# Kernel tuning notes

Hardware: AMD Instinct MI355X
Metric: run time of the kernel (lower is better)

Reference implementation:

```python
import jax, jax.numpy as jnp
import numpy as np

ALPHA = 0.9
BETA = 0.85
THRESHOLD = 0.1
SURR_SCALE = 100.0  # SpyTorch-style surrogate gradient scale


@jax.custom_vjp
def surr_spike(x):
    # Heaviside forward, surrogate gradient backward (SurrGradSpike)
    return (x > 0.0).astype(x.dtype)


def _surr_fwd(x):
    return surr_spike(x), x


def _surr_bwd(x, g):
    return (g / (SURR_SCALE * jnp.abs(x) + 1.0) ** 2,)


surr_spike.defvjp(_surr_fwd, _surr_bwd)


def setup_inputs() -> dict:
    key = jax.random.key(0)
    k1, k2, k3 = jax.random.split(key, 3)
    B, T, D_IN, N = 64, 256, 512, 1024
    inputs = jax.random.normal(k1, (B, T, D_IN), dtype=jnp.float32)
    weights = 0.1 * jax.random.normal(k2, (D_IN, N), dtype=jnp.float32)
    recurrent_weights = 0.1 * jax.random.normal(k3, (N, N), dtype=jnp.float32)
    return {"inputs": inputs, "weights": weights, "recurrent_weights": recurrent_weights}


def reference(inputs, weights, recurrent_weights):
    B, T, D_IN = inputs.shape
    N = weights.shape[1]

    def step(carry, x_t):
        mem, syn, spk = carry
        h = jnp.einsum('bd,dn->bn', x_t, weights)          # input projection
        rec_h = jnp.einsum('bn,nm->bm', spk, recurrent_weights)  # recurrent drive
        new_syn = ALPHA * syn + h + rec_h
        new_mem = BETA * mem + new_syn
        mthr = new_mem - THRESHOLD
        out = surr_spike(mthr)
        new_mem = jnp.where(mthr > 0.0, jnp.zeros_like(new_mem), new_mem)  # reset
        return (new_mem, new_syn, out), (out, new_mem, new_syn)

    zeros = jnp.zeros((B, N), dtype=inputs.dtype)
    init = (zeros, zeros, zeros)
    x_tbd = jnp.transpose(inputs, (1, 0, 2))  # [T, B, D]
    (mem, syn, spk), (spk_rec, mem_rec, syn_rec) = jax.lax.scan(step, init, x_tbd)
    # back to [B, T, N]
    spk_rec = jnp.transpose(spk_rec, (1, 0, 2))
    mem_rec = jnp.transpose(mem_rec, (1, 0, 2))
    syn_rec = jnp.transpose(syn_rec, (1, 0, 2))
    return (spk_rec, (mem, syn, spk), (mem_rec, syn_rec))
```

## Files before the change

### kernel.cpp

```cpp
#include <hip/hip_runtime.h>

typedef __attribute__((ext_vector_type(8))) _Float16 f16x8;
typedef __attribute__((ext_vector_type(4))) float f32x4;

static constexpr int   B_  = 64;
static constexpr int   T_  = 256;
static constexpr int   D_  = 512;
static constexpr int   N_  = 1024;
static constexpr float ALPHA_ = 0.9f;
static constexpr float BETA_  = 0.85f;
static constexpr float THR_   = 0.1f;
static constexpr float INV4096 = 1.0f / 4096.0f;

__global__ __launch_bounds__(256) void dsrnn_wsplit(const float* __restrict__ W,
                                                    unsigned char* __restrict__ Wfrag) {
  const int u    = blockIdx.x * 256 + threadIdx.x;
  const int lane = u & 63;
  const int bi   = u >> 6;
  const int cf   = bi >> 4;
  const int chk  = bi & 15;
  const int kg   = lane >> 4;
  const int cc   = lane & 15;
  const int n    = cf * 16 + cc;
  const int k0   = chk * 32 + kg * 8;
  f16x8 vh, vl;
#pragma unroll
  for (int j = 0; j < 8; ++j) {
    const float v = W[(size_t)(k0 + j) * N_ + n];
    const _Float16 h = (_Float16)v;
    vh[j] = h;
    vl[j] = (_Float16)((v - (float)h) * 4096.0f);
  }
  unsigned char* dst = Wfrag + (size_t)bi * 2048 + lane * 16;
  *reinterpret_cast<f16x8*>(dst)        = vh;
  *reinterpret_cast<f16x8*>(dst + 1024) = vl;
}

__global__ __launch_bounds__(256) void dsrnn_hgemm2(const float* __restrict__ X,
                                                    const unsigned char* __restrict__ Wfrag,
                                                    float* __restrict__ H) {
  __shared__ __align__(16) _Float16 Xa_hi[64][40];
  __shared__ __align__(16) _Float16 Xa_lo[64][40];
  const int tid  = threadIdx.x;
  const int rb   = blockIdx.x >> 3;
  const int nb   = (blockIdx.x & 7) << 7;
  const int r0   = rb << 6;
  const int wv   = tid >> 6;
  const int lane = tid & 63;
  const int kg   = lane >> 4;
  const int cc   = lane & 15;

  f32x4 ah[4][2], am[4][2];
#pragma unroll
  for (int i = 0; i < 4; ++i)
#pragma unroll
    for (int j = 0; j < 2; ++j) {
      ah[i][j] = (f32x4){0.f, 0.f, 0.f, 0.f};
      am[i][j] = (f32x4){0.f, 0.f, 0.f, 0.f};
    }

  const int srow = tid >> 2;
  const int skq  = (tid & 3) << 3;

  for (int kc = 0; kc < 16; ++kc) {
    {
      const float* xp = X + (size_t)(r0 + srow) * D_ + kc * 32 + skq;
      const float4 v0 = *reinterpret_cast<const float4*>(xp);
      const float4 v1 = *reinterpret_cast<const float4*>(xp + 4);
      const float vv[8] = {v0.x, v0.y, v0.z, v0.w, v1.x, v1.y, v1.z, v1.w};
      f16x8 xh, xl;
#pragma unroll
      for (int j = 0; j < 8; ++j) {
        const _Float16 h = (_Float16)vv[j];
        xh[j] = h;
        xl[j] = (_Float16)((vv[j] - (float)h) * 4096.0f);
      }
      *reinterpret_cast<f16x8*>(&Xa_hi[srow][skq]) = xh;
      *reinterpret_cast<f16x8*>(&Xa_lo[srow][skq]) = xl;
    }
    __syncthreads();

    f16x8 Bh[2], Bl[2];
#pragma unroll
    for (int cfi = 0; cfi < 2; ++cfi) {
      const unsigned char* bp =
          Wfrag + (size_t)((((nb >> 4) + (wv << 1) + cfi) * 16 + kc) * 2048) + lane * 16;
      Bh[cfi] = *reinterpret_cast<const f16x8*>(bp);
      Bl[cfi] = *reinterpret_cast<const f16x8*>(bp + 1024);
    }

#pragma unroll
    for (int rf = 0; rf < 4; ++rf) {
      const f16x8 Ah = *reinterpret_cast<const f16x8*>(&Xa_hi[rf * 16 + cc][kg * 8]);
      const f16x8 Al = *reinterpret_cast<const f16x8*>(&Xa_lo[rf * 16 + cc][kg * 8]);
#pragma unroll
      for (int cfi = 0; cfi < 2; ++cfi) {
        ah[rf][cfi] = __builtin_amdgcn_mfma_f32_16x16x32_f16(Ah, Bh[cfi], ah[rf][cfi], 0, 0, 0);
        am[rf][cfi] = __builtin_amdgcn_mfma_f32_16x16x32_f16(Ah, Bl[cfi], am[rf][cfi], 0, 0, 0);
        am[rf][cfi] = __builtin_amdgcn_mfma_f32_16x16x32_f16(Al, Bh[cfi], am[rf][cfi], 0, 0, 0);
      }
    }
    __syncthreads();
  }

#pragma unroll
  for (int rf = 0; rf < 4; ++rf)
#pragma unroll
    for (int cfi = 0; cfi < 2; ++cfi) {
      const int col = nb + wv * 32 + cfi * 16 + cc;
#pragma unroll
      for (int rr = 0; rr < 4; ++rr) {
        const int row = r0 + rf * 16 + kg * 4 + rr;
        H[(size_t)row * N_ + col] = fmaf(am[rf][cfi][rr], INV4096, ah[rf][cfi][rr]);
      }
    }
}

__global__ __launch_bounds__(256, 1) void dsrnn_step10(
    const float* __restrict__ Rw,
    float* __restrict__ spk_rec,
    float* __restrict__ mem_rec,
    float* __restrict__ syn_rec,
    float* __restrict__ mem_fin,
    float* __restrict__ syn_fin,
    float* __restrict__ spk_fin,
    unsigned long long* masks)
{
  extern __shared__ unsigned char RsB[];
  __shared__ unsigned smaskU[16][33];
  __shared__ float scratch[4][512];

  const int tid  = threadIdx.x;
  const int bq   = blockIdx.x >> 5;
  const int mg   = blockIdx.x & 31;
  const int wv   = tid >> 6;
  const int lane = tid & 63;
  const int kg   = lane >> 4;
  const int cc   = lane & 15;

  for (int k = 0; k < 128; ++k) {
    const int e  = (k << 8) + tid;
    const int n  = e >> 5;
    const int ml = e & 31;
    const float v = Rw[(size_t)n * N_ + (mg << 5) + ml];
    const _Float16 hi = (_Float16)v;
    const float hif = (float)hi;
    const _Float16 lo = (_Float16)((v - hif) * 4096.0f);
    const int s   = n >> 5;
    const int kin = n & 31;
    const int ln  = ((kin >> 3) << 4) + (ml & 15);
    const int mt  = ml >> 4;
    const int off = ((((s << 1) + mt) << 1) << 10) + (ln << 4) + ((kin & 7) << 1);
    *(_Float16*)(RsB + off)        = hi;
    *(_Float16*)(RsB + off + 1024) = lo;
  }

  const int bl1 = tid >> 5;
  const int bl2 = bl1 + 8;
  const int ml_ = tid & 31;
  const int b1  = (bq << 4) + bl1;
  const int b2  = (bq << 4) + bl2;
  const int m   = (mg << 5) + ml_;

  float mem1 = 0.f, syn1 = 0.f, spv1 = 0.f;
  float mem2 = 0.f, syn2 = 0.f, spv2 = 0.f;
  float po1s = 0.f, po1m = 0.f, po1y = 0.f;
  float po2s = 0.f, po2m = 0.f, po2y = 0.f;

  __syncthreads();

  for (int t = 0; t < T_; ++t) {
    const size_t i1 = ((size_t)b1 * T_ + t) * N_ + m;
    const size_t i2 = ((size_t)b2 * T_ + t) * N_ + m;
    const float h1 = syn_rec[i1];
    const float h2 = syn_rec[i2];

    {
      unsigned long long* base = masks + (size_t)(t & 1) * 2048;
      unsigned long long* p1 = base + (size_t)b1 * 32 + ml_;
      unsigned long long* p2 = base + (size_t)b2 * 32 + ml_;
      unsigned long long w1 =
          __hip_atomic_load(p1, __ATOMIC_RELAXED, __HIP_MEMORY_SCOPE_AGENT);
      unsigned long long w2 =
          __hip_atomic_load(p2, __ATOMIC_RELAXED, __HIP_MEMORY_SCOPE_AGENT);
      int g = 0;
      while ((((unsigned)(w1 >> 32) != (unsigned)t) |
              ((unsigned)(w2 >> 32) != (unsigned)t)) && ++g < (1 << 20)) {
        __builtin_amdgcn_s_sleep(1);
        w1 = __hip_atomic_load(p1, __ATOMIC_RELAXED, __HIP_MEMORY_SCOPE_AGENT);
        w2 = __hip_atomic_load(p2, __ATOMIC_RELAXED, __HIP_MEMORY_SCOPE_AGENT);
      }
      smaskU[bl1][ml_] = (unsigned)w1;
      smaskU[bl2][ml_] = (unsigned)w2;
    }

    if (t > 0) {
      spk_rec[i1 - N_] = po1s; mem_rec[i1 - N_] = po1m; syn_rec[i1 - N_] = po1y;
      spk_rec[i2 - N_] = po2s; mem_rec[i2 - N_] = po2m; syn_rec[i2 - N_] = po2y;
    }
    __syncthreads();

    f32x4 c0h = {0.f, 0.f, 0.f, 0.f};
    f32x4 c0l = {0.f, 0.f, 0.f, 0.f};
    f32x4 c1h = {0.f, 0.f, 0.f, 0.f};
    f32x4 c1l = {0.f, 0.f, 0.f, 0.f};
    const int shB = kg << 3;
#pragma unroll
    for (int ss = 0; ss < 8; ++ss) {
      const int s = (wv << 3) + ss;
      const unsigned bits8 = (smaskU[cc][s] >> shB) & 0xFFu;
      union { unsigned u[4]; f16x8 v; } A;
#pragma unroll
      for (int p = 0; p < 4; ++p) {
        const unsigned e0 = (bits8 >> (2 * p)) & 1u;
        const unsigned e1 = (bits8 >> (2 * p + 1)) & 1u;
        A.u[p] = e0 * 0x3C00u + e1 * 0x3C000000u;
      }
      const unsigned char* sb = RsB + (s << 12) + (lane << 4);
      const f16x8 b00 = *reinterpret_cast<const f16x8*>(sb);
      const f16x8 b01 = *reinterpret_cast<const f16x8*>(sb + 1024);
      const f16x8 b10 = *reinterpret_cast<const f16x8*>(sb + 2048);
      const f16x8 b11 = *reinterpret_cast<const f16x8*>(sb + 3072);
      c0h = __builtin_amdgcn_mfma_f32_16x16x32_f16(A.v, b00, c0h, 0, 0, 0);
      c0l = __builtin_amdgcn_mfma_f32_16x16x32_f16(A.v, b01, c0l, 0, 0, 0);
      c1h = __builtin_amdgcn_mfma_f32_16x16x32_f16(A.v, b10, c1h, 0, 0, 0);
      c1l = __builtin_amdgcn_mfma_f32_16x16x32_f16(A.v, b11, c1l, 0, 0, 0);
    }
#pragma unroll
    for (int r = 0; r < 4; ++r) {
      const int row = (kg << 2) + r;
      scratch[wv][(row << 5) + cc]      = fmaf(c0l[r], INV4096, c0h[r]);
      scratch[wv][(row << 5) + cc + 16] = fmaf(c1l[r], INV4096, c1h[r]);
    }
    __syncthreads();

    const int o1 = (bl1 << 5) + ml_;
    const int o2 = (bl2 << 5) + ml_;
    const float rec1 =
        scratch[0][o1] + scratch[1][o1] + scratch[2][o1] + scratch[3][o1];
    const float rec2 =
        scratch[0][o2] + scratch[1][o2] + scratch[2][o2] + scratch[3][o2];

    syn1 = ALPHA_ * syn1 + h1 + rec1;
    mem1 = BETA_ * mem1 + syn1;
    const bool sp1 = (mem1 - THR_) > 0.f;
    spv1 = sp1 ? 1.f : 0.f;
    mem1 = sp1 ? 0.f : mem1;

    syn2 = ALPHA_ * syn2 + h2 + rec2;
    mem2 = BETA_ * mem2 + syn2;
    const bool sp2 = (mem2 - THR_) > 0.f;
    spv2 = sp2 ? 1.f : 0.f;
    mem2 = sp2 ? 0.f : mem2;

    const unsigned long long ball1 = __ballot(sp1);
    const unsigned long long ball2 = __ballot(sp2);
    if (ml_ == 0) {
      const unsigned sh = lane & 32;
      const unsigned long long tag = ((unsigned long long)(unsigned)(t + 1)) << 32;
      unsigned long long* nb = masks + (size_t)((t + 1) & 1) * 2048;
      __hip_atomic_store(nb + (size_t)b1 * 32 + mg,
                         tag | (unsigned)(ball1 >> sh),
                         __ATOMIC_RELAXED, __HIP_MEMORY_SCOPE_AGENT);
      __hip_atomic_store(nb + (size_t)b2 * 32 + mg,
                         tag | (unsigned)(ball2 >> sh),
                         __ATOMIC_RELAXED, __HIP_MEMORY_SCOPE_AGENT);
    }

    po1s = spv1; po1m = mem1; po1y = syn1;
    po2s = spv2; po2m = mem2; po2y = syn2;
  }

  const size_t l1 = ((size_t)b1 * T_ + (T_ - 1)) * N_ + m;
  const size_t l2 = ((size_t)b2 * T_ + (T_ - 1)) * N_ + m;
  spk_rec[l1] = po1s; mem_rec[l1] = po1m; syn_rec[l1] = po1y;
  spk_rec[l2] = po2s; mem_rec[l2] = po2m; syn_rec[l2] = po2y;
  mem_fin[b1 * N_ + m] = mem1; syn_fin[b1 * N_ + m] = syn1; spk_fin[b1 * N_ + m] = spv1;
  mem_fin[b2 * N_ + m] = mem2; syn_fin[b2 * N_ + m] = syn2; spk_fin[b2 * N_ + m] = spv2;
}

extern "C" void kernel_launch(void* const* d_in, const int* in_sizes, int n_in,
                              void* d_out, int out_size, void* d_ws, size_t ws_size,
                              hipStream_t stream) {
  const float* X  = (const float*)d_in[0];
  const float* W  = (const float*)d_in[1];
  const float* Rw = (const float*)d_in[2];

  float* out = (float*)d_out;
  const size_t BTN = (size_t)B_ * T_ * N_;
  const size_t BN  = (size_t)B_ * N_;
  float* spk_rec = out;
  float* mem_fin = out + BTN;
  float* syn_fin = mem_fin + BN;
  float* spk_fin = syn_fin + BN;
  float* mem_rec = spk_fin + BN;
  float* syn_rec = mem_rec + BTN;

  unsigned char* Wfrag = (unsigned char*)mem_rec;

  unsigned long long* masks = (unsigned long long*)d_ws;
  hipMemsetAsync(d_ws, 0, (size_t)2 * 64 * 32 * sizeof(unsigned long long), stream);

  dsrnn_wsplit<<<dim3(256), dim3(256), 0, stream>>>(W, Wfrag);
  dsrnn_hgemm2<<<dim3(2048), dim3(256), 0, stream>>>(X, Wfrag, syn_rec);

  (void)hipFuncSetAttribute((const void*)dsrnn_step10,
                            hipFuncAttributeMaxDynamicSharedMemorySize, 131072);
  void* args[] = {(void*)&Rw,      (void*)&spk_rec, (void*)&mem_rec,
                  (void*)&syn_rec, (void*)&mem_fin, (void*)&syn_fin,
                  (void*)&spk_fin, (void*)&masks};
  hipLaunchCooperativeKernel((void*)dsrnn_step10, dim3(128), dim3(256), args,
                             131072, stream);
}
```

Baseline: 769.8 us.

## Remove per-step barrier by polling spike masks per wave and shuffling

Each wave now polls only the two mask words it needs for its own K-slice and spreads them across lanes with __shfl. This replaces the shared smaskU staging and the first __syncthreads of each timestep. The scratch reduction buffer is double-buffered by timestep parity so a single barrier per step stays race-free. Output records are written right after compute instead of being deferred one step. This removes one block-wide barrier from the serial critical path, at the cost of shuffle instructions and more lanes polling global memory.

```diff
diff --git a/kernel.cpp b/kernel.cpp
--- a/kernel.cpp
+++ b/kernel.cpp
@@ -116,7 +116,7 @@
     }
 }
 
-__global__ __launch_bounds__(256, 1) void dsrnn_step10(
+__global__ __launch_bounds__(256, 1) void dsrnn_step11(
     const float* __restrict__ Rw,
     float* __restrict__ spk_rec,
     float* __restrict__ mem_rec,
@@ -127,8 +127,7 @@
     unsigned long long* masks)
 {
   extern __shared__ unsigned char RsB[];
-  __shared__ unsigned smaskU[16][33];
-  __shared__ float scratch[4][512];
+  __shared__ float scratch[2][4][512];
 
   const int tid  = threadIdx.x;
   const int bq   = blockIdx.x >> 5;
@@ -162,10 +161,10 @@
   const int b2  = (bq << 4) + bl2;
   const int m   = (mg << 5) + ml_;
 
+  const int pw_off = ((bq << 4) + cc) * 32 + (wv << 3) + (kg << 1);
+
   float mem1 = 0.f, syn1 = 0.f, spv1 = 0.f;
   float mem2 = 0.f, syn2 = 0.f, spv2 = 0.f;
-  float po1s = 0.f, po1m = 0.f, po1y = 0.f;
-  float po2s = 0.f, po2m = 0.f, po2y = 0.f;
 
   __syncthreads();
 
@@ -175,30 +174,23 @@
     const float h1 = syn_rec[i1];
     const float h2 = syn_rec[i2];
 
+    unsigned pay0, pay1;
     {
-      unsigned long long* base = masks + (size_t)(t & 1) * 2048;
-      unsigned long long* p1 = base + (size_t)b1 * 32 + ml_;
-      unsigned long long* p2 = base + (size_t)b2 * 32 + ml_;
+      unsigned long long* p0 = masks + (size_t)(t & 1) * 2048 + pw_off;
+      unsigned long long w0 =
+          __hip_atomic_load(p0,     __ATOMIC_RELAXED, __HIP_MEMORY_SCOPE_AGENT);
       unsigned long long w1 =
-          __hip_atomic_load(p1, __ATOMIC_RELAXED, __HIP_MEMORY_SCOPE_AGENT);
-      unsigned long long w2 =
-          __hip_atomic_load(p2, __ATOMIC_RELAXED, __HIP_MEMORY_SCOPE_AGENT);
+          __hip_atomic_load(p0 + 1, __ATOMIC_RELAXED, __HIP_MEMORY_SCOPE_AGENT);
       int g = 0;
-      while ((((unsigned)(w1 >> 32) != (unsigned)t) |
-              ((unsigned)(w2 >> 32) != (unsigned)t)) && ++g < (1 << 20)) {
+      while ((((unsigned)(w0 >> 32) != (unsigned)t) |
+              ((unsigned)(w1 >> 32) != (unsigned)t)) && ++g < (1 << 20)) {
         __builtin_amdgcn_s_sleep(1);
-        w1 = __hip_atomic_load(p1, __ATOMIC_RELAXED, __HIP_MEMORY_SCOPE_AGENT);
-        w2 = __hip_atomic_load(p2, __ATOMIC_RELAXED, __HIP_MEMORY_SCOPE_AGENT);
-      }
-      smaskU[bl1][ml_] = (unsigned)w1;
-      smaskU[bl2][ml_] = (unsigned)w2;
-    }
-
-    if (t > 0) {
-      spk_rec[i1 - N_] = po1s; mem_rec[i1 - N_] = po1m; syn_rec[i1 - N_] = po1y;
-      spk_rec[i2 - N_] = po2s; mem_rec[i2 - N_] = po2m; syn_rec[i2 - N_] = po2y;
-    }
-    __syncthreads();
+        w0 = __hip_atomic_load(p0,     __ATOMIC_RELAXED, __HIP_MEMORY_SCOPE_AGENT);
+        w1 = __hip_atomic_load(p0 + 1, __ATOMIC_RELAXED, __HIP_MEMORY_SCOPE_AGENT);
+      }
+      pay0 = (unsigned)w0;
+      pay1 = (unsigned)w1;
+    }
 
     f32x4 c0h = {0.f, 0.f, 0.f, 0.f};
     f32x4 c0l = {0.f, 0.f, 0.f, 0.f};
@@ -207,8 +199,9 @@
     const int shB = kg << 3;
 #pragma unroll
     for (int ss = 0; ss < 8; ++ss) {
-      const int s = (wv << 3) + ss;
-      const unsigned bits8 = (smaskU[cc][s] >> shB) & 0xFFu;
+      const int srcl = cc + ((ss >> 1) << 4);
+      const unsigned word = __shfl((ss & 1) ? pay1 : pay0, srcl, 64);
+      const unsigned bits8 = (word >> shB) & 0xFFu;
       union { unsigned u[4]; f16x8 v; } A;
 #pragma unroll
       for (int p = 0; p < 4; ++p) {
@@ -216,6 +209,7 @@
         const unsigned e1 = (bits8 >> (2 * p + 1)) & 1u;
         A.u[p] = e0 * 0x3C00u + e1 * 0x3C000000u;
       }
+      const int s = (wv << 3) + ss;
       const unsigned char* sb = RsB + (s << 12) + (lane << 4);
       const f16x8 b00 = *reinterpret_cast<const f16x8*>(sb);
       const f16x8 b01 = *reinterpret_cast<const f16x8*>(sb + 1024);
@@ -226,20 +220,22 @@
       c1h = __builtin_amdgcn_mfma_f32_16x16x32_f16(A.v, b10, c1h, 0, 0, 0);
       c1l = __builtin_amdgcn_mfma_f32_16x16x32_f16(A.v, b11, c1l, 0, 0, 0);
     }
-#pragma unroll
-    for (int r = 0; r < 4; ++r) {
-      const int row = (kg << 2) + r;
-      scratch[wv][(row << 5) + cc]      = fmaf(c0l[r], INV4096, c0h[r]);
-      scratch[wv][(row << 5) + cc + 16] = fmaf(c1l[r], INV4096, c1h[r]);
+    {
+      float* scr = &scratch[t & 1][wv][0];
+#pragma unroll
+      for (int r = 0; r < 4; ++r) {
+        const int row = (kg << 2) + r;
+        scr[(row << 5) + cc]      = fmaf(c0l[r], INV4096, c0h[r]);
+        scr[(row << 5) + cc + 16] = fmaf(c1l[r], INV4096, c1h[r]);
+      }
     }
     __syncthreads();
 
+    const float* sc = &scratch[t & 1][0][0];
     const int o1 = (bl1 << 5) + ml_;
     const int o2 = (bl2 << 5) + ml_;
-    const float rec1 =
-        scratch[0][o1] + scratch[1][o1] + scratch[2][o1] + scratch[3][o1];
-    const float rec2 =
-        scratch[0][o2] + scratch[1][o2] + scratch[2][o2] + scratch[3][o2];
+    const float rec1 = sc[o1] + sc[512 + o1] + sc[1024 + o1] + sc[1536 + o1];
+    const float rec2 = sc[o2] + sc[512 + o2] + sc[1024 + o2] + sc[1536 + o2];
 
     syn1 = ALPHA_ * syn1 + h1 + rec1;
     mem1 = BETA_ * mem1 + syn1;
@@ -267,14 +263,10 @@
                          __ATOMIC_RELAXED, __HIP_MEMORY_SCOPE_AGENT);
     }
 
-    po1s = spv1; po1m = mem1; po1y = syn1;
-    po2s = spv2; po2m = mem2; po2y = syn2;
+    spk_rec[i1] = spv1; mem_rec[i1] = mem1; syn_rec[i1] = syn1;
+    spk_rec[i2] = spv2; mem_rec[i2] = mem2; syn_rec[i2] = syn2;
   }
 
-  const size_t l1 = ((size_t)b1 * T_ + (T_ - 1)) * N_ + m;
-  const size_t l2 = ((size_t)b2 * T_ + (T_ - 1)) * N_ + m;
-  spk_rec[l1] = po1s; mem_rec[l1] = po1m; syn_rec[l1] = po1y;
-  spk_rec[l2] = po2s; mem_rec[l2] = po2m; syn_rec[l2] = po2y;
   mem_fin[b1 * N_ + m] = mem1; syn_fin[b1 * N_ + m] = syn1; spk_fin[b1 * N_ + m] = spv1;
   mem_fin[b2 * N_ + m] = mem2; syn_fin[b2 * N_ + m] = syn2; spk_fin[b2 * N_ + m] = spv2;
 }
@@ -304,11 +296,11 @@
   dsrnn_wsplit<<<dim3(256), dim3(256), 0, stream>>>(W, Wfrag);
   dsrnn_hgemm2<<<dim3(2048), dim3(256), 0, stream>>>(X, Wfrag, syn_rec);
 
-  (void)hipFuncSetAttribute((const void*)dsrnn_step10,
+  (void)hipFuncSetAttribute((const void*)dsrnn_step11,
                             hipFuncAttributeMaxDynamicSharedMemorySize, 131072);
   void* args[] = {(void*)&Rw,      (void*)&spk_rec, (void*)&mem_rec,
                   (void*)&syn_rec, (void*)&mem_fin, (void*)&syn_fin,
                   (void*)&spk_fin, (void*)&masks};
-  hipLaunchCooperativeKernel((void*)dsrnn_step10, dim3(128), dim3(256), args,
+  hipLaunchCooperativeKernel((void*)dsrnn_step11, dim3(128), dim3(256), args,
                              131072, stream);
 }
```

Result: slower. 946.6 us (+23.0%).
